# Kernel tuning notes

Hardware: AMD Instinct MI355X
Metric: run time of the kernel (lower is better)

## Reference

```python
import jax, jax.numpy as jnp
import numpy as np
import math

C_IN = 1024
C = 64
N_HEAD = 16
B, S = 4, 1024


def setup_inputs() -> dict:
    key = jax.random.key(0)
    ks = jax.random.split(key, 8)
    scale = 1.0 / math.sqrt(C_IN)
    x = jax.random.normal(ks[0], (B, S, C_IN), dtype=jnp.float32)
    bias = jax.random.normal(ks[1], (B, N_HEAD, S, S), dtype=jnp.float32) * 0.1
    attention_mask = jax.random.randint(ks[2], (B, S), 0, 2, dtype=jnp.int32)
    Wq = jax.random.normal(ks[3], (C_IN, C * N_HEAD), dtype=jnp.float32) * scale
    Wk = jax.random.normal(ks[4], (C_IN, C * N_HEAD), dtype=jnp.float32) * scale
    Wv = jax.random.normal(ks[5], (C_IN, C * N_HEAD), dtype=jnp.float32) * scale
    Wo = jax.random.normal(ks[6], (C * N_HEAD, C_IN), dtype=jnp.float32) * scale
    bo = jax.random.normal(ks[7], (C_IN,), dtype=jnp.float32) * 0.01
    return {"x": x, "bias": bias, "attention_mask": attention_mask,
            "Wq": Wq, "Wk": Wk, "Wv": Wv, "Wo": Wo, "bo": bo}


def reference(x, bias, attention_mask, Wq, Wk, Wv, Wo, bo):
    # x: (B, S, c_in); attn_dim=1 so the attention axis is already at -2.
    q = x @ Wq  # (B, S, H*c)
    k = x @ Wk
    v = x @ Wv
    # split heads: (B, S, H, c) -> (B, H, S, c)
    def split_heads(t):
        return t.reshape(t.shape[:-1] + (N_HEAD, C)).swapaxes(-2, -3)
    q, k, v = split_heads(q), split_heads(k), split_heads(v)
    q = q / math.sqrt(C)
    a = jnp.einsum('bhqc,bhkc->bhqk', q, k)  # (B, H, S, S)
    a = a + bias
    offset = jnp.where(attention_mask[:, None, None, :] == 0, -1e8, 0.0).astype(a.dtype)
    a = a + offset
    a = jax.nn.softmax(a, axis=-1)
    o = jnp.einsum('bhqk,bhkc->bhqc', a, v)  # (B, H, S, c)
    o = o.swapaxes(-3, -2).reshape(B, S, N_HEAD * C)
    out = o @ Wo + bo  # (B, S, c_in)
    return out
```

## Files before the change

### kernel.cpp

```cpp
#include <hip/hip_runtime.h>
#include <hip/hip_bf16.h>
#include <math.h>

#define B_   4
#define S_   1024
#define CIN  1024
#define H_   16
#define CH   64
#define HC   1024

typedef __bf16 bf16;
typedef __bf16 bf16x8 __attribute__((ext_vector_type(8)));
typedef __bf16 bf16x4 __attribute__((ext_vector_type(4)));
typedef float  f32x4  __attribute__((ext_vector_type(4)));

__device__ __forceinline__ void gld16(const bf16* g, bf16* l) {
  __builtin_amdgcn_global_load_lds(
      (const __attribute__((address_space(1))) unsigned int*)g,
      (__attribute__((address_space(3))) unsigned int*)l,
      16, 0, 0);
}

__global__ __launch_bounds__(256) void cast_x_kernel(const float* __restrict__ x,
                                                     bf16* __restrict__ xb) {
  int i = (blockIdx.x * 256 + threadIdx.x) * 4;
  f32x4 v = *(const f32x4*)(x + i);
  bf16x4 o;
  o[0] = (bf16)v[0]; o[1] = (bf16)v[1]; o[2] = (bf16)v[2]; o[3] = (bf16)v[3];
  *(bf16x4*)(xb + i) = o;
}

__global__ __launch_bounds__(256) void transW_kernel(
    const float* __restrict__ Wq, const float* __restrict__ Wk,
    const float* __restrict__ Wv, const float* __restrict__ Wo,
    bf16* __restrict__ Wqt, bf16* __restrict__ Wkt,
    bf16* __restrict__ Wvt, bf16* __restrict__ Wot) {
  const float* W; bf16* Wt;
  switch (blockIdx.z) {
    case 0: W = Wq; Wt = Wqt; break;
    case 1: W = Wk; Wt = Wkt; break;
    case 2: W = Wv; Wt = Wvt; break;
    default: W = Wo; Wt = Wot; break;
  }
  __shared__ float tile[64][65];
  const int r0 = blockIdx.y * 64, c0 = blockIdx.x * 64;
  const int tx = threadIdx.x & 63, ty = threadIdx.x >> 6;
#pragma unroll
  for (int j = 0; j < 64; j += 4)
    tile[ty + j][tx] = W[(size_t)(r0 + ty + j) * 1024 + c0 + tx];
  __syncthreads();
#pragma unroll
  for (int j = 0; j < 64; j += 4)
    Wt[(size_t)(c0 + ty + j) * 1024 + r0 + tx] = (bf16)tile[tx][ty + j];
}

template <int MODE>
__global__ __launch_bounds__(256) void gemm_kernel(
    const bf16* __restrict__ A, const bf16* __restrict__ Bt,
    bf16* __restrict__ outb, float* __restrict__ outf,
    const float* __restrict__ bo, float scale) {
  __shared__ bf16 Asm[128 * 32];
  __shared__ bf16 Bsm[128 * 32];
  const int tid = threadIdx.x;
  const int lane = tid & 63, wave = tid >> 6;
  const int m0 = blockIdx.y * 128, n0 = blockIdx.x * 128;
  const int wr = wave >> 1, wc = wave & 1;
  const int K = 1024;

  f32x4 acc[4][4] = {};

  const int srow = tid >> 2;
  const int scol = (tid & 3) * 8;
  const size_t abase = (size_t)(m0 + srow) * K + scol;
  const size_t bbase = (size_t)(n0 + srow) * K + scol;
  bf16* lA = Asm + wave * 512;
  bf16* lB = Bsm + wave * 512;

  for (int kt = 0; kt < K; kt += 32) {
    gld16(A + abase + kt, lA);
    gld16(A + abase + (size_t)64 * K + kt, lA + 2048);
    gld16(Bt + bbase + kt, lB);
    gld16(Bt + bbase + (size_t)64 * K + kt, lB + 2048);
    __syncthreads();
    bf16x8 af[4], bfr[4];
#pragma unroll
    for (int m = 0; m < 4; m++)
      af[m] = *(const bf16x8*)(Asm + (wr * 64 + m * 16 + (lane & 15)) * 32 + (lane >> 4) * 8);
#pragma unroll
    for (int n = 0; n < 4; n++)
      bfr[n] = *(const bf16x8*)(Bsm + (wc * 64 + n * 16 + (lane & 15)) * 32 + (lane >> 4) * 8);
#pragma unroll
    for (int m = 0; m < 4; m++)
#pragma unroll
      for (int n = 0; n < 4; n++)
        acc[m][n] = __builtin_amdgcn_mfma_f32_16x16x32_bf16(af[m], bfr[n], acc[m][n], 0, 0, 0);
    __syncthreads();
  }

#pragma unroll
  for (int m = 0; m < 4; m++) {
#pragma unroll
    for (int n = 0; n < 4; n++) {
      const int col = n0 + wc * 64 + n * 16 + (lane & 15);
      const int grow = m0 + wr * 64 + m * 16 + (lane >> 4) * 4;
      if (MODE == 0) {
        const int h = col >> 6, c = col & 63;
#pragma unroll
        for (int r = 0; r < 4; r++) {
          const int gr = grow + r;
          const int b = gr >> 10, s = gr & 1023;
          outb[(((size_t)b * H_ + h) * S_ + s) * CH + c] = (bf16)(acc[m][n][r] * scale);
        }
      } else {
        const float bv = bo[col];
#pragma unroll
        for (int r = 0; r < 4; r++)
          outf[(size_t)(grow + r) * 1024 + col] = acc[m][n][r] + bv;
      }
    }
  }
}

__global__ __launch_bounds__(256) void vtrans_kernel(const bf16* __restrict__ V,
                                                     bf16* __restrict__ Vt) {
  const int bh = blockIdx.y;
  const int s0 = blockIdx.x * 64;
  __shared__ bf16 tile[64][72];
  const int tid = threadIdx.x;
  const int row = tid >> 2;
  const int col = (tid & 3) * 16;
  const bf16* src = V + (size_t)bh * S_ * CH;
  bf16* dst = Vt + (size_t)bh * CH * S_;
  *(bf16x8*)&tile[row][col]     = *(const bf16x8*)(src + (size_t)(s0 + row) * CH + col);
  *(bf16x8*)&tile[row][col + 8] = *(const bf16x8*)(src + (size_t)(s0 + row) * CH + col + 8);
  __syncthreads();
  bf16x8 o0, o1;
#pragma unroll
  for (int j = 0; j < 8; j++) { o0[j] = tile[col + j][row]; o1[j] = tile[col + 8 + j][row]; }
  *(bf16x8*)(dst + (size_t)row * S_ + s0 + col)     = o0;
  *(bf16x8*)(dst + (size_t)row * S_ + s0 + col + 8) = o1;
}

__global__ __launch_bounds__(256) void attn_kernel(
    const bf16* __restrict__ Q, const bf16* __restrict__ Ka,
    const bf16* __restrict__ Vt, const float* __restrict__ bias,
    const int* __restrict__ mask, bf16* __restrict__ O) {
  const int bh = blockIdx.y, b = bh >> 4, h = bh & 15;
  const int q0 = blockIdx.x * 64;
  const int tid = threadIdx.x, wave = tid >> 6, lane = tid & 63;
  const int qr = lane & 15, kg = lane >> 4;
  __shared__ bf16 Ksm[64][72];
  __shared__ bf16 Vsm[64][72];
  __shared__ bf16 Psm[4][16][72];

  const bf16* Qp = Q + ((size_t)bh * S_ + q0 + wave * 16 + qr) * CH;
  bf16x8 qf[2];
  qf[0] = *(const bf16x8*)(Qp + kg * 8);
  qf[1] = *(const bf16x8*)(Qp + 32 + kg * 8);

  f32x4 oacc[4] = {};
  float mrow[4] = {-1e30f, -1e30f, -1e30f, -1e30f};
  float lrow[4] = {0.f, 0.f, 0.f, 0.f};

  const float* biasp = bias + ((size_t)bh * S_ + q0 + wave * 16 + kg * 4) * S_;
  const int* maskp = mask + b * S_;
  const bf16* Kp = Ka + (size_t)bh * S_ * CH;
  const bf16* Vp = Vt + (size_t)bh * CH * S_;

  const int srow = tid >> 2, scol = (tid & 3) * 16;

  for (int k0 = 0; k0 < S_; k0 += 64) {
    *(bf16x8*)&Ksm[srow][scol]     = *(const bf16x8*)(Kp + (size_t)(k0 + srow) * CH + scol);
    *(bf16x8*)&Ksm[srow][scol + 8] = *(const bf16x8*)(Kp + (size_t)(k0 + srow) * CH + scol + 8);
    *(bf16x8*)&Vsm[srow][scol]     = *(const bf16x8*)(Vp + (size_t)srow * S_ + k0 + scol);
    *(bf16x8*)&Vsm[srow][scol + 8] = *(const bf16x8*)(Vp + (size_t)srow * S_ + k0 + scol + 8);
    __syncthreads();

    f32x4 sf[4] = {};
#pragma unroll
    for (int n = 0; n < 4; n++) {
#pragma unroll
      for (int j = 0; j < 2; j++) {
        bf16x8 kf = *(const bf16x8*)&Ksm[n * 16 + qr][j * 32 + kg * 8];
        sf[n] = __builtin_amdgcn_mfma_f32_16x16x32_bf16(qf[j], kf, sf[n], 0, 0, 0);
      }
    }
#pragma unroll
    for (int n = 0; n < 4; n++) {
      const int col = k0 + n * 16 + qr;
      const float moff = (maskp[col] == 0) ? -1e8f : 0.0f;
#pragma unroll
      for (int r = 0; r < 4; r++)
        sf[n][r] += biasp[(size_t)r * S_ + col] + moff;
    }
#pragma unroll
    for (int r = 0; r < 4; r++) {
      float tm = fmaxf(fmaxf(sf[0][r], sf[1][r]), fmaxf(sf[2][r], sf[3][r]));
      tm = fmaxf(tm, __shfl_xor(tm, 1));
      tm = fmaxf(tm, __shfl_xor(tm, 2));
      tm = fmaxf(tm, __shfl_xor(tm, 4));
      tm = fmaxf(tm, __shfl_xor(tm, 8));
      const float nm = fmaxf(mrow[r], tm);
      const float al = __expf(mrow[r] - nm);
      mrow[r] = nm;
      float rs = 0.f;
#pragma unroll
      for (int n = 0; n < 4; n++) {
        const float p = __expf(sf[n][r] - nm);
        sf[n][r] = p;
        rs += p;
      }
      rs += __shfl_xor(rs, 1);
      rs += __shfl_xor(rs, 2);
      rs += __shfl_xor(rs, 4);
      rs += __shfl_xor(rs, 8);
      lrow[r] = lrow[r] * al + rs;
#pragma unroll
      for (int n = 0; n < 4; n++) oacc[n][r] *= al;
    }
#pragma unroll
    for (int n = 0; n < 4; n++)
#pragma unroll
      for (int r = 0; r < 4; r++)
        Psm[wave][kg * 4 + r][n * 16 + qr] = (bf16)sf[n][r];
    __asm__ volatile("s_waitcnt lgkmcnt(0)" ::: "memory");
#pragma unroll
    for (int n = 0; n < 4; n++) {
#pragma unroll
      for (int j = 0; j < 2; j++) {
        bf16x8 pf = *(const bf16x8*)&Psm[wave][qr][j * 32 + kg * 8];
        bf16x8 vf = *(const bf16x8*)&Vsm[n * 16 + qr][j * 32 + kg * 8];
        oacc[n] = __builtin_amdgcn_mfma_f32_16x16x32_bf16(pf, vf, oacc[n], 0, 0, 0);
      }
    }
    __syncthreads();
  }
#pragma unroll
  for (int r = 0; r < 4; r++) {
    const float inv = 1.0f / lrow[r];
    const int s = q0 + wave * 16 + kg * 4 + r;
#pragma unroll
    for (int n = 0; n < 4; n++)
      O[((size_t)b * S_ + s) * HC + h * CH + n * 16 + qr] = (bf16)(oacc[n][r] * inv);
  }
}

extern "C" void kernel_launch(void* const* d_in, const int* in_sizes, int n_in,
                              void* d_out, int out_size, void* d_ws, size_t ws_size,
                              hipStream_t stream) {
  (void)in_sizes; (void)n_in; (void)out_size; (void)ws_size;
  const float* x    = (const float*)d_in[0];
  const float* bias = (const float*)d_in[1];
  const int*   mask = (const int*)d_in[2];
  const float* Wq   = (const float*)d_in[3];
  const float* Wk   = (const float*)d_in[4];
  const float* Wv   = (const float*)d_in[5];
  const float* Wo   = (const float*)d_in[6];
  const float* bo   = (const float*)d_in[7];
  float* out = (float*)d_out;

  char* ws = (char*)d_ws;
  bf16* xb  = (bf16*)(ws);
  bf16* Wqt = (bf16*)(ws + (8u  << 20));
  bf16* Wkt = (bf16*)(ws + (10u << 20));
  bf16* Wvt = (bf16*)(ws + (12u << 20));
  bf16* Wot = (bf16*)(ws + (14u << 20));
  bf16* Qa  = (bf16*)(ws + (16u << 20));
  bf16* Kaa = (bf16*)(ws + (24u << 20));
  bf16* Va  = (bf16*)(ws + (32u << 20));
  bf16* Vtr = (bf16*)(ws + (40u << 20));
  bf16* Oa  = (bf16*)(ws + (48u << 20));

  cast_x_kernel<<<4096, 256, 0, stream>>>(x, xb);
  transW_kernel<<<dim3(16, 16, 4), 256, 0, stream>>>(Wq, Wk, Wv, Wo, Wqt, Wkt, Wvt, Wot);
  gemm_kernel<0><<<dim3(8, 32), 256, 0, stream>>>(xb, Wqt, Qa, nullptr, nullptr, 0.125f);
  gemm_kernel<0><<<dim3(8, 32), 256, 0, stream>>>(xb, Wkt, Kaa, nullptr, nullptr, 1.0f);
  gemm_kernel<0><<<dim3(8, 32), 256, 0, stream>>>(xb, Wvt, Va, nullptr, nullptr, 1.0f);
  vtrans_kernel<<<dim3(16, 64), 256, 0, stream>>>(Va, Vtr);
  attn_kernel<<<dim3(16, 64), 256, 0, stream>>>(Qa, Kaa, Vtr, bias, mask, Oa);
  gemm_kernel<1><<<dim3(8, 32), 256, 0, stream>>>(Oa, Wot, nullptr, out, bo, 1.0f);
}
```

Baseline: 528.0 us.

## Fuse QKV projections into one GEMM, write V transposed, prefetch bias tiles

The Q, K and V projections become one GEMM over a concatenated weight matrix, launched once with a three-times-wider grid. The epilogue writes V directly in transposed layout, which removes the separate vtrans kernel and its extra pass over V. The attention kernel now stages bias tiles through shared memory with coalesced float4 loads, prefetches the next K/V/bias tile into registers while computing the current one, and precomputes the mask offsets into shared memory. MFMA sections are wrapped in s_setprio, and the added shared-memory buffers raise LDS use, which may lower occupancy.

```diff
diff --git a/kernel.cpp b/kernel.cpp
--- a/kernel.cpp
+++ b/kernel.cpp
@@ -33,13 +33,12 @@
 __global__ __launch_bounds__(256) void transW_kernel(
     const float* __restrict__ Wq, const float* __restrict__ Wk,
     const float* __restrict__ Wv, const float* __restrict__ Wo,
-    bf16* __restrict__ Wqt, bf16* __restrict__ Wkt,
-    bf16* __restrict__ Wvt, bf16* __restrict__ Wot) {
+    bf16* __restrict__ Wqkvt, bf16* __restrict__ Wot) {
   const float* W; bf16* Wt;
   switch (blockIdx.z) {
-    case 0: W = Wq; Wt = Wqt; break;
-    case 1: W = Wk; Wt = Wkt; break;
-    case 2: W = Wv; Wt = Wvt; break;
+    case 0: W = Wq; Wt = Wqkvt; break;
+    case 1: W = Wk; Wt = Wqkvt + (size_t)1024 * 1024; break;
+    case 2: W = Wv; Wt = Wqkvt + (size_t)2048 * 1024; break;
     default: W = Wo; Wt = Wot; break;
   }
   __shared__ float tile[64][65];
@@ -57,8 +56,8 @@
 template <int MODE>
 __global__ __launch_bounds__(256) void gemm_kernel(
     const bf16* __restrict__ A, const bf16* __restrict__ Bt,
-    bf16* __restrict__ outb, float* __restrict__ outf,
-    const float* __restrict__ bo, float scale) {
+    bf16* __restrict__ Qa, bf16* __restrict__ Ka, bf16* __restrict__ Vt,
+    float* __restrict__ outf, const float* __restrict__ bo) {
   __shared__ bf16 Asm[128 * 32];
   __shared__ bf16 Bsm[128 * 32];
   const int tid = threadIdx.x;
@@ -89,11 +88,13 @@
 #pragma unroll
     for (int n = 0; n < 4; n++)
       bfr[n] = *(const bf16x8*)(Bsm + (wc * 64 + n * 16 + (lane & 15)) * 32 + (lane >> 4) * 8);
+    __builtin_amdgcn_s_setprio(1);
 #pragma unroll
     for (int m = 0; m < 4; m++)
 #pragma unroll
       for (int n = 0; n < 4; n++)
         acc[m][n] = __builtin_amdgcn_mfma_f32_16x16x32_bf16(af[m], bfr[n], acc[m][n], 0, 0, 0);
+    __builtin_amdgcn_s_setprio(0);
     __syncthreads();
   }
 
@@ -104,12 +105,24 @@
       const int col = n0 + wc * 64 + n * 16 + (lane & 15);
       const int grow = m0 + wr * 64 + m * 16 + (lane >> 4) * 4;
       if (MODE == 0) {
-        const int h = col >> 6, c = col & 63;
-#pragma unroll
-        for (int r = 0; r < 4; r++) {
-          const int gr = grow + r;
-          const int b = gr >> 10, s = gr & 1023;
-          outb[(((size_t)b * H_ + h) * S_ + s) * CH + c] = (bf16)(acc[m][n][r] * scale);
+        const int which = col >> 10;
+        const int hcol = col & 1023, hh = hcol >> 6, cc = hcol & 63;
+        const int bb = grow >> 10, s0v = grow & 1023;
+        if (which == 0) {
+          const size_t base = (((size_t)bb * H_ + hh) * S_ + s0v) * CH + cc;
+#pragma unroll
+          for (int r = 0; r < 4; r++)
+            Qa[base + (size_t)r * CH] = (bf16)(acc[m][n][r] * 0.125f);
+        } else if (which == 1) {
+          const size_t base = (((size_t)bb * H_ + hh) * S_ + s0v) * CH + cc;
+#pragma unroll
+          for (int r = 0; r < 4; r++)
+            Ka[base + (size_t)r * CH] = (bf16)acc[m][n][r];
+        } else {
+          bf16x4 pv;
+#pragma unroll
+          for (int r = 0; r < 4; r++) pv[r] = (bf16)acc[m][n][r];
+          *(bf16x4*)(Vt + (((size_t)bb * H_ + hh) * CH + cc) * S_ + s0v) = pv;
         }
       } else {
         const float bv = bo[col];
@@ -119,26 +132,6 @@
       }
     }
   }
-}
-
-__global__ __launch_bounds__(256) void vtrans_kernel(const bf16* __restrict__ V,
-                                                     bf16* __restrict__ Vt) {
-  const int bh = blockIdx.y;
-  const int s0 = blockIdx.x * 64;
-  __shared__ bf16 tile[64][72];
-  const int tid = threadIdx.x;
-  const int row = tid >> 2;
-  const int col = (tid & 3) * 16;
-  const bf16* src = V + (size_t)bh * S_ * CH;
-  bf16* dst = Vt + (size_t)bh * CH * S_;
-  *(bf16x8*)&tile[row][col]     = *(const bf16x8*)(src + (size_t)(s0 + row) * CH + col);
-  *(bf16x8*)&tile[row][col + 8] = *(const bf16x8*)(src + (size_t)(s0 + row) * CH + col + 8);
-  __syncthreads();
-  bf16x8 o0, o1;
-#pragma unroll
-  for (int j = 0; j < 8; j++) { o0[j] = tile[col + j][row]; o1[j] = tile[col + 8 + j][row]; }
-  *(bf16x8*)(dst + (size_t)row * S_ + s0 + col)     = o0;
-  *(bf16x8*)(dst + (size_t)row * S_ + s0 + col + 8) = o1;
 }
 
 __global__ __launch_bounds__(256) void attn_kernel(
@@ -149,9 +142,22 @@
   const int q0 = blockIdx.x * 64;
   const int tid = threadIdx.x, wave = tid >> 6, lane = tid & 63;
   const int qr = lane & 15, kg = lane >> 4;
+
   __shared__ bf16 Ksm[64][72];
   __shared__ bf16 Vsm[64][72];
   __shared__ bf16 Psm[4][16][72];
+  __shared__ float Bsm[64][68];
+  __shared__ float Msm[S_];
+
+  {
+    const int4 mv = *(const int4*)(mask + (size_t)b * S_ + tid * 4);
+    f32x4 mo;
+    mo[0] = (mv.x == 0) ? -1e8f : 0.f;
+    mo[1] = (mv.y == 0) ? -1e8f : 0.f;
+    mo[2] = (mv.z == 0) ? -1e8f : 0.f;
+    mo[3] = (mv.w == 0) ? -1e8f : 0.f;
+    *(f32x4*)(Msm + tid * 4) = mo;
+  }
 
   const bf16* Qp = Q + ((size_t)bh * S_ + q0 + wave * 16 + qr) * CH;
   bf16x8 qf[2];
@@ -162,21 +168,51 @@
   float mrow[4] = {-1e30f, -1e30f, -1e30f, -1e30f};
   float lrow[4] = {0.f, 0.f, 0.f, 0.f};
 
-  const float* biasp = bias + ((size_t)bh * S_ + q0 + wave * 16 + kg * 4) * S_;
-  const int* maskp = mask + b * S_;
   const bf16* Kp = Ka + (size_t)bh * S_ * CH;
   const bf16* Vp = Vt + (size_t)bh * CH * S_;
+  const float* biasT = bias + ((size_t)bh * S_ + q0) * S_;
 
   const int srow = tid >> 2, scol = (tid & 3) * 16;
-
-  for (int k0 = 0; k0 < S_; k0 += 64) {
-    *(bf16x8*)&Ksm[srow][scol]     = *(const bf16x8*)(Kp + (size_t)(k0 + srow) * CH + scol);
-    *(bf16x8*)&Ksm[srow][scol + 8] = *(const bf16x8*)(Kp + (size_t)(k0 + srow) * CH + scol + 8);
-    *(bf16x8*)&Vsm[srow][scol]     = *(const bf16x8*)(Vp + (size_t)srow * S_ + k0 + scol);
-    *(bf16x8*)&Vsm[srow][scol + 8] = *(const bf16x8*)(Vp + (size_t)srow * S_ + k0 + scol + 8);
+  const int brow = tid >> 4, bcol = (tid & 15) * 4;
+
+  bf16x8 kr0, kr1, vr0, vr1;
+  f32x4 brg[4];
+
+  {
+    const int k0 = 0;
+    kr0 = *(const bf16x8*)(Kp + (size_t)(k0 + srow) * CH + scol);
+    kr1 = *(const bf16x8*)(Kp + (size_t)(k0 + srow) * CH + scol + 8);
+    vr0 = *(const bf16x8*)(Vp + (size_t)srow * S_ + k0 + scol);
+    vr1 = *(const bf16x8*)(Vp + (size_t)srow * S_ + k0 + scol + 8);
+#pragma unroll
+    for (int i = 0; i < 4; i++)
+      brg[i] = *(const f32x4*)(biasT + (size_t)(brow + i * 16) * S_ + k0 + bcol);
+  }
+
+  for (int t = 0; t < S_ / 64; t++) {
+    const int k0 = t * 64;
     __syncthreads();
+    *(bf16x8*)&Ksm[srow][scol] = kr0;
+    *(bf16x8*)&Ksm[srow][scol + 8] = kr1;
+    *(bf16x8*)&Vsm[srow][scol] = vr0;
+    *(bf16x8*)&Vsm[srow][scol + 8] = vr1;
+#pragma unroll
+    for (int i = 0; i < 4; i++)
+      *(f32x4*)&Bsm[brow + i * 16][bcol] = brg[i];
+    if (t + 1 < S_ / 64) {
+      const int kn = k0 + 64;
+      kr0 = *(const bf16x8*)(Kp + (size_t)(kn + srow) * CH + scol);
+      kr1 = *(const bf16x8*)(Kp + (size_t)(kn + srow) * CH + scol + 8);
+      vr0 = *(const bf16x8*)(Vp + (size_t)srow * S_ + kn + scol);
+      vr1 = *(const bf16x8*)(Vp + (size_t)srow * S_ + kn + scol + 8);
+#pragma unroll
+      for (int i = 0; i < 4; i++)
+        brg[i] = *(const f32x4*)(biasT + (size_t)(brow + i * 16) * S_ + kn + bcol);
+    }
+    __syncthreads();
 
     f32x4 sf[4] = {};
+    __builtin_amdgcn_s_setprio(1);
 #pragma unroll
     for (int n = 0; n < 4; n++) {
 #pragma unroll
@@ -185,13 +221,13 @@
         sf[n] = __builtin_amdgcn_mfma_f32_16x16x32_bf16(qf[j], kf, sf[n], 0, 0, 0);
       }
     }
+    __builtin_amdgcn_s_setprio(0);
 #pragma unroll
     for (int n = 0; n < 4; n++) {
-      const int col = k0 + n * 16 + qr;
-      const float moff = (maskp[col] == 0) ? -1e8f : 0.0f;
+      const float moff = Msm[k0 + n * 16 + qr];
 #pragma unroll
       for (int r = 0; r < 4; r++)
-        sf[n][r] += biasp[(size_t)r * S_ + col] + moff;
+        sf[n][r] += Bsm[wave * 16 + kg * 4 + r][n * 16 + qr] + moff;
     }
 #pragma unroll
     for (int r = 0; r < 4; r++) {
@@ -224,6 +260,7 @@
       for (int r = 0; r < 4; r++)
         Psm[wave][kg * 4 + r][n * 16 + qr] = (bf16)sf[n][r];
     __asm__ volatile("s_waitcnt lgkmcnt(0)" ::: "memory");
+    __builtin_amdgcn_s_setprio(1);
 #pragma unroll
     for (int n = 0; n < 4; n++) {
 #pragma unroll
@@ -233,7 +270,7 @@
         oacc[n] = __builtin_amdgcn_mfma_f32_16x16x32_bf16(pf, vf, oacc[n], 0, 0, 0);
       }
     }
-    __syncthreads();
+    __builtin_amdgcn_s_setprio(0);
   }
 #pragma unroll
   for (int r = 0; r < 4; r++) {
@@ -260,23 +297,17 @@
   float* out = (float*)d_out;
 
   char* ws = (char*)d_ws;
-  bf16* xb  = (bf16*)(ws);
-  bf16* Wqt = (bf16*)(ws + (8u  << 20));
-  bf16* Wkt = (bf16*)(ws + (10u << 20));
-  bf16* Wvt = (bf16*)(ws + (12u << 20));
-  bf16* Wot = (bf16*)(ws + (14u << 20));
-  bf16* Qa  = (bf16*)(ws + (16u << 20));
-  bf16* Kaa = (bf16*)(ws + (24u << 20));
-  bf16* Va  = (bf16*)(ws + (32u << 20));
-  bf16* Vtr = (bf16*)(ws + (40u << 20));
-  bf16* Oa  = (bf16*)(ws + (48u << 20));
+  bf16* xb    = (bf16*)(ws);
+  bf16* Wqkvt = (bf16*)(ws + (8u  << 20));
+  bf16* Wot   = (bf16*)(ws + (14u << 20));
+  bf16* Qa    = (bf16*)(ws + (16u << 20));
+  bf16* Kaa   = (bf16*)(ws + (24u << 20));
+  bf16* Vtr   = (bf16*)(ws + (32u << 20));
+  bf16* Oa    = (bf16*)(ws + (40u << 20));
 
   cast_x_kernel<<<4096, 256, 0, stream>>>(x, xb);
-  transW_kernel<<<dim3(16, 16, 4), 256, 0, stream>>>(Wq, Wk, Wv, Wo, Wqt, Wkt, Wvt, Wot);
-  gemm_kernel<0><<<dim3(8, 32), 256, 0, stream>>>(xb, Wqt, Qa, nullptr, nullptr, 0.125f);
-  gemm_kernel<0><<<dim3(8, 32), 256, 0, stream>>>(xb, Wkt, Kaa, nullptr, nullptr, 1.0f);
-  gemm_kernel<0><<<dim3(8, 32), 256, 0, stream>>>(xb, Wvt, Va, nullptr, nullptr, 1.0f);
-  vtrans_kernel<<<dim3(16, 64), 256, 0, stream>>>(Va, Vtr);
+  transW_kernel<<<dim3(16, 16, 4), 256, 0, stream>>>(Wq, Wk, Wv, Wo, Wqkvt, Wot);
+  gemm_kernel<0><<<dim3(24, 32), 256, 0, stream>>>(xb, Wqkvt, Qa, Kaa, Vtr, nullptr, nullptr);
   attn_kernel<<<dim3(16, 64), 256, 0, stream>>>(Qa, Kaa, Vtr, bias, mask, Oa);
-  gemm_kernel<1><<<dim3(8, 32), 256, 0, stream>>>(Oa, Wot, nullptr, out, bo, 1.0f);
-}
+  gemm_kernel<1><<<dim3(8, 32), 256, 0, stream>>>(Oa, Wot, nullptr, nullptr, nullptr, out, bo);
+}
```

Result: faster. 489.7 us (-7.2%).
